# Performance work log

Hardware: AMD Instinct MI355X
Metric: run time of the kernel (lower is better)

## Reference

```python
import jax, jax.numpy as jnp
import numpy as np


def setup_inputs() -> dict:
    key = jax.random.key(0)
    k1, k2 = jax.random.split(key)
    B, M, N = 4, 8192, 8192
    pc_src = jax.random.normal(k1, (B, 3, M), dtype=jnp.float32)
    pc_dst = jax.random.normal(k2, (B, 3, N), dtype=jnp.float32)
    return {"pc_src": pc_src, "pc_dst": pc_dst}


def reference(pc_src, pc_dst):
    # pc_src: [B, 3, M], pc_dst: [B, 3, N]
    # Pairwise squared L2 via ||a||^2 + ||b||^2 - 2 a.b (avoids [B,3,M,N] diff tensor)
    src_sq = jnp.sum(pc_src * pc_src, axis=1)          # [B, M]
    dst_sq = jnp.sum(pc_dst * pc_dst, axis=1)          # [B, N]
    cross = jnp.einsum('bdm,bdn->bmn', pc_src, pc_dst)  # [B, M, N]
    d2 = src_sq[:, :, None] + dst_sq[:, None, :] - 2.0 * cross
    dist = jnp.sqrt(jnp.maximum(d2, 0.0))               # [B, M, N]
    min_dist = jnp.min(dist, axis=2)                     # [B, M]
    return jnp.mean(min_dist)
```

## Files before the change

kernel.cpp:

```cpp
#include <hip/hip_runtime.h>
#include <math.h>


#define TPB 256

constexpr int NB = 4;
constexpr int NM = 8192;
constexpr int NN = 8192;
constexpr int NPTS = NB * NM;
constexpr int NSEG = 16;
constexpr int DSEG = NN / NSEG;
constexpr int TILES = DSEG / 32;
constexpr int NSRCG = NM / 512;
constexpr int FIN_TPB = 128;
constexpr int NBLK_F = NPTS / FIN_TPB;

typedef _Float16 half8 __attribute__((ext_vector_type(8)));
typedef float f32x16 __attribute__((ext_vector_type(16)));

__device__ __forceinline__ float min3(float a, float b, float c) {
    return fminf(fminf(a, b), c);
}
__device__ __forceinline__ float tile_min(const f32x16& c, float acc) {
    float v0 = min3(c[0],  c[1],  c[2]);
    float v1 = min3(c[3],  c[4],  c[5]);
    float v2 = min3(c[6],  c[7],  c[8]);
    float v3 = min3(c[9],  c[10], c[11]);
    float v4 = min3(c[12], c[13], c[14]);
    float w0 = min3(v0, v1, c[15]);
    float w1 = min3(v2, v3, v4);
    return min3(acc, w0, w1);
}
__device__ __forceinline__ int aidx(int r, int h) {
    return ((r << 1) | h) ^ ((r >> 2) & 7);
}

__global__ __launch_bounds__(TPB) void minseg_kernel(const float* __restrict__ src,
                                                     const float* __restrict__ dst,
                                                     float* __restrict__ part,
                                                     unsigned long long* __restrict__ sumfix,
                                                     unsigned* __restrict__ ticket) {
    __shared__ uint4 alds[DSEG * 2];

    int l  = threadIdx.x & 63;
    int wv = threadIdx.x >> 6;
    int sg = blockIdx.x & (NSEG - 1);
    int b  = (blockIdx.x >> 4) & 3;
    int srcgrp = blockIdx.x >> 6;

    if (blockIdx.x == 0 && threadIdx.x == 0) { *sumfix = 0ULL; *ticket = 0u; }

    const float* pd = dst + (size_t)b * 3 * NN;
#pragma unroll
    for (int rr = 0; rr < 2; ++rr) {
        int r = threadIdx.x + rr * TPB;
        int n = sg * DSEG + r;
        float x = pd[n], y = pd[NN + n], z = pd[2 * NN + n];
        float ux = -2.0f * x, uy = -2.0f * y, uz = -2.0f * z;
        float w = fmaf(x, x, fmaf(y, y, z * z));
        _Float16 uhx = (_Float16)ux; _Float16 ulx = (_Float16)(ux - (float)uhx);
        _Float16 uhy = (_Float16)uy; _Float16 uly = (_Float16)(uy - (float)uhy);
        _Float16 uhz = (_Float16)uz; _Float16 ulz = (_Float16)(uz - (float)uhz);
        _Float16 wh  = (_Float16)w;  _Float16 wl  = (_Float16)(w - (float)wh);
        half8 a0 = {uhx, uhx, ulx, uhy, uhy, uly, uhz, uhz};
        half8 a1 = {ulz, wh, wl, (_Float16)0.f, (_Float16)0.f,
                    (_Float16)0.f, (_Float16)0.f, (_Float16)0.f};
        alds[aidx(r, 0)] = *(uint4*)&a0;
        alds[aidx(r, 1)] = *(uint4*)&a1;
    }

    int mbase = (srcgrp * 4 + wv) * 128;
    int lg = l & 31;
    int hi = l >> 5;
    const float* ps = src + (size_t)b * 3 * NM;
    half8 bf[4];
#pragma unroll
    for (int k = 0; k < 4; ++k) {
        int c = mbase + k * 32 + lg;
        float x = ps[c], y = ps[NM + c], z = ps[2 * NM + c];
        _Float16 shx = (_Float16)x; _Float16 slx = (_Float16)(x - (float)shx);
        _Float16 shy = (_Float16)y; _Float16 sly = (_Float16)(y - (float)shy);
        _Float16 shz = (_Float16)z; _Float16 slz = (_Float16)(z - (float)shz);
        half8 b0 = {shx, slx, shx, shy, sly, shy, shz, slz};
        half8 b1 = {shz, (_Float16)1.f, (_Float16)1.f, (_Float16)0.f,
                    (_Float16)0.f, (_Float16)0.f, (_Float16)0.f, (_Float16)0.f};
        bf[k] = hi ? b1 : b0;
    }
    __syncthreads();

    const f32x16 zc = {0.f,0.f,0.f,0.f,0.f,0.f,0.f,0.f,
                       0.f,0.f,0.f,0.f,0.f,0.f,0.f,0.f};
    float acc0 = 3.4e38f, acc1 = 3.4e38f, acc2 = 3.4e38f, acc3 = 3.4e38f;
#pragma unroll 2
    for (int j = 0; j < TILES; ++j) {
        uint4 av = alds[aidx(j * 32 + lg, hi)];
        half8 af = *(half8*)&av;
        f32x16 c0 = __builtin_amdgcn_mfma_f32_32x32x16_f16(af, bf[0], zc, 0, 0, 0);
        acc0 = tile_min(c0, acc0);
        f32x16 c1 = __builtin_amdgcn_mfma_f32_32x32x16_f16(af, bf[1], zc, 0, 0, 0);
        acc1 = tile_min(c1, acc1);
        f32x16 c2 = __builtin_amdgcn_mfma_f32_32x32x16_f16(af, bf[2], zc, 0, 0, 0);
        acc2 = tile_min(c2, acc2);
        f32x16 c3 = __builtin_amdgcn_mfma_f32_32x32x16_f16(af, bf[3], zc, 0, 0, 0);
        acc3 = tile_min(c3, acc3);
    }

    acc0 = fminf(acc0, __shfl_xor(acc0, 32));
    acc1 = fminf(acc1, __shfl_xor(acc1, 32));
    acc2 = fminf(acc2, __shfl_xor(acc2, 32));
    acc3 = fminf(acc3, __shfl_xor(acc3, 32));

    float* pp = part + (size_t)sg * NPTS + b * NM + mbase;
    int lo = (l < 32);
    pp[lo ? lg      : 32 + lg] = lo ? acc0 : acc1;
    pp[lo ? 64 + lg : 96 + lg] = lo ? acc2 : acc3;
}

__global__ __launch_bounds__(FIN_TPB) void finish_kernel(const float* __restrict__ src,
                                                         const float* __restrict__ part,
                                                         unsigned long long* __restrict__ sumfix,
                                                         unsigned* __restrict__ ticket,
                                                         float* __restrict__ out) {
    int gm = blockIdx.x * FIN_TPB + threadIdx.x;
    int b = gm / NM, m = gm % NM;

    float v = fminf(part[gm], part[NPTS + gm]);
#pragma unroll
    for (int s = 2; s < NSEG; s += 2)
        v = min3(v, part[(size_t)s * NPTS + gm], part[(size_t)(s + 1) * NPTS + gm]);

    const float* sp = src + (size_t)b * 3 * NM;
    float x = sp[m], y = sp[NM + m], z = sp[2 * NM + m];
    float a2 = fmaf(x, x, fmaf(y, y, z * z));
    float d = sqrtf(fmaxf(a2 + v, 0.0f));

    for (int off = 32; off > 0; off >>= 1) d += __shfl_down(d, off);
    __shared__ float wsum[2];
    int lane = threadIdx.x & 63, w = threadIdx.x >> 6;
    if (lane == 0) wsum[w] = d;
    __syncthreads();

    if (threadIdx.x == 0) {
        float bs = wsum[0] + wsum[1];
        unsigned long long inc = (unsigned long long)((double)bs * 4294967296.0);
        atomicAdd(sumfix, inc);
        __threadfence();
        unsigned tk = atomicAdd(ticket, 1u);
        if (tk == NBLK_F - 1) {
            unsigned long long tot = atomicAdd(sumfix, 0ULL);
            out[0] = (float)((double)tot * (1.0 / 4294967296.0) * (1.0 / NPTS));
        }
    }
}

extern "C" void kernel_launch(void* const* d_in, const int* in_sizes, int n_in,
                              void* d_out, int out_size, void* d_ws, size_t ws_size,
                              hipStream_t stream) {
    const float* src = (const float*)d_in[0];
    const float* dst = (const float*)d_in[1];
    float* out = (float*)d_out;

    char* ws = (char*)d_ws;
    float* part = (float*)ws;
    unsigned long long* sumfix =
        (unsigned long long*)(ws + (size_t)NSEG * NPTS * 4);
    unsigned* ticket = (unsigned*)(ws + (size_t)NSEG * NPTS * 4 + 8);

    minseg_kernel<<<NSEG * NB * NSRCG, TPB, 0, stream>>>(src, dst, part,
                                                         sumfix, ticket);
    finish_kernel<<<NBLK_F, FIN_TPB, 0, stream>>>(src, part, sumfix, ticket, out);
}
```

Baseline: 27.62 us.

## Fuse finish reduction into min kernel via per-group last-block tickets

Result: slower. 94.72 us (+243.0%).

```diff
diff --git a/kernel.cpp b/kernel.cpp
--- a/kernel.cpp
+++ b/kernel.cpp
@@ -12,8 +12,7 @@
 constexpr int DSEG = NN / NSEG;
 constexpr int TILES = DSEG / 32;
 constexpr int NSRCG = NM / 512;
-constexpr int FIN_TPB = 128;
-constexpr int NBLK_F = NPTS / FIN_TPB;
+constexpr int NGRP = NB * NSRCG;
 
 typedef _Float16 half8 __attribute__((ext_vector_type(8)));
 typedef float f32x16 __attribute__((ext_vector_type(16)));
@@ -35,20 +34,22 @@
     return ((r << 1) | h) ^ ((r >> 2) & 7);
 }
 
-__global__ __launch_bounds__(TPB) void minseg_kernel(const float* __restrict__ src,
-                                                     const float* __restrict__ dst,
-                                                     float* __restrict__ part,
-                                                     unsigned long long* __restrict__ sumfix,
-                                                     unsigned* __restrict__ ticket) {
+__global__ __launch_bounds__(TPB) void fused_kernel(const float* __restrict__ src,
+                                                    const float* __restrict__ dst,
+                                                    float* __restrict__ part,
+                                                    unsigned* __restrict__ tg,
+                                                    unsigned long long* __restrict__ sumfix,
+                                                    unsigned* __restrict__ ticket,
+                                                    float* __restrict__ out) {
     __shared__ uint4 alds[DSEG * 2];
+    __shared__ int sfold;
+    __shared__ float wsum[4];
 
     int l  = threadIdx.x & 63;
     int wv = threadIdx.x >> 6;
     int sg = blockIdx.x & (NSEG - 1);
     int b  = (blockIdx.x >> 4) & 3;
     int srcgrp = blockIdx.x >> 6;
-
-    if (blockIdx.x == 0 && threadIdx.x == 0) { *sumfix = 0ULL; *ticket = 0u; }
 
     const float* pd = dst + (size_t)b * 3 * NN;
 #pragma unroll
@@ -112,41 +113,57 @@
 
     float* pp = part + (size_t)sg * NPTS + b * NM + mbase;
     int lo = (l < 32);
-    pp[lo ? lg      : 32 + lg] = lo ? acc0 : acc1;
-    pp[lo ? 64 + lg : 96 + lg] = lo ? acc2 : acc3;
-}
-
-__global__ __launch_bounds__(FIN_TPB) void finish_kernel(const float* __restrict__ src,
-                                                         const float* __restrict__ part,
-                                                         unsigned long long* __restrict__ sumfix,
-                                                         unsigned* __restrict__ ticket,
-                                                         float* __restrict__ out) {
-    int gm = blockIdx.x * FIN_TPB + threadIdx.x;
-    int b = gm / NM, m = gm % NM;
-
-    float v = fminf(part[gm], part[NPTS + gm]);
-#pragma unroll
-    for (int s = 2; s < NSEG; s += 2)
-        v = min3(v, part[(size_t)s * NPTS + gm], part[(size_t)(s + 1) * NPTS + gm]);
-
-    const float* sp = src + (size_t)b * 3 * NM;
-    float x = sp[m], y = sp[NM + m], z = sp[2 * NM + m];
-    float a2 = fmaf(x, x, fmaf(y, y, z * z));
-    float d = sqrtf(fmaxf(a2 + v, 0.0f));
-
-    for (int off = 32; off > 0; off >>= 1) d += __shfl_down(d, off);
-    __shared__ float wsum[2];
-    int lane = threadIdx.x & 63, w = threadIdx.x >> 6;
-    if (lane == 0) wsum[w] = d;
+    __hip_atomic_store(&pp[lo ? lg : 32 + lg], lo ? acc0 : acc1,
+                       __ATOMIC_RELAXED, __HIP_MEMORY_SCOPE_AGENT);
+    __hip_atomic_store(&pp[lo ? 64 + lg : 96 + lg], lo ? acc2 : acc3,
+                       __ATOMIC_RELAXED, __HIP_MEMORY_SCOPE_AGENT);
+    __threadfence();
     __syncthreads();
 
     if (threadIdx.x == 0) {
-        float bs = wsum[0] + wsum[1];
+        unsigned old = __hip_atomic_fetch_add(&tg[b * NSRCG + srcgrp], 1u,
+                                              __ATOMIC_ACQ_REL,
+                                              __HIP_MEMORY_SCOPE_AGENT);
+        sfold = (old == NSEG - 1);
+    }
+    __syncthreads();
+    if (!sfold) return;
+
+    int gbase = b * NM + srcgrp * 512;
+    const float* sp = src + (size_t)b * 3 * NM;
+    float dsum = 0.0f;
+#pragma unroll
+    for (int cc = 0; cc < 2; ++cc) {
+        int c = threadIdx.x + cc * TPB;
+        int gm = gbase + c;
+        float v = fminf(
+            __hip_atomic_load(&part[gm], __ATOMIC_RELAXED, __HIP_MEMORY_SCOPE_AGENT),
+            __hip_atomic_load(&part[NPTS + gm], __ATOMIC_RELAXED, __HIP_MEMORY_SCOPE_AGENT));
+#pragma unroll
+        for (int s = 2; s < NSEG; s += 2) {
+            float va = __hip_atomic_load(&part[(size_t)s * NPTS + gm],
+                                         __ATOMIC_RELAXED, __HIP_MEMORY_SCOPE_AGENT);
+            float vb = __hip_atomic_load(&part[(size_t)(s + 1) * NPTS + gm],
+                                         __ATOMIC_RELAXED, __HIP_MEMORY_SCOPE_AGENT);
+            v = min3(v, va, vb);
+        }
+        int m = srcgrp * 512 + c;
+        float x = sp[m], y = sp[NM + m], z = sp[2 * NM + m];
+        float a2 = fmaf(x, x, fmaf(y, y, z * z));
+        dsum += sqrtf(fmaxf(a2 + v, 0.0f));
+    }
+
+    for (int off = 32; off > 0; off >>= 1) dsum += __shfl_down(dsum, off);
+    if (l == 0) wsum[wv] = dsum;
+    __syncthreads();
+
+    if (threadIdx.x == 0) {
+        float bs = (wsum[0] + wsum[1]) + (wsum[2] + wsum[3]);
         unsigned long long inc = (unsigned long long)((double)bs * 4294967296.0);
         atomicAdd(sumfix, inc);
         __threadfence();
         unsigned tk = atomicAdd(ticket, 1u);
-        if (tk == NBLK_F - 1) {
+        if (tk == NGRP - 1) {
             unsigned long long tot = atomicAdd(sumfix, 0ULL);
             out[0] = (float)((double)tot * (1.0 / 4294967296.0) * (1.0 / NPTS));
         }
@@ -162,11 +179,12 @@
 
     char* ws = (char*)d_ws;
     float* part = (float*)ws;
-    unsigned long long* sumfix =
-        (unsigned long long*)(ws + (size_t)NSEG * NPTS * 4);
-    unsigned* ticket = (unsigned*)(ws + (size_t)NSEG * NPTS * 4 + 8);
+    char* ctrl = ws + (size_t)NSEG * NPTS * 4;
+    unsigned* tg = (unsigned*)ctrl;
+    unsigned long long* sumfix = (unsigned long long*)(ctrl + 256);
+    unsigned* ticket = (unsigned*)(ctrl + 264);
 
-    minseg_kernel<<<NSEG * NB * NSRCG, TPB, 0, stream>>>(src, dst, part,
-                                                         sumfix, ticket);
-    finish_kernel<<<NBLK_F, FIN_TPB, 0, stream>>>(src, part, sumfix, ticket, out);
+    hipMemsetAsync(ctrl, 0, 272, stream);
+    fused_kernel<<<NSEG * NB * NSRCG, TPB, 0, stream>>>(src, dst, part, tg,
+                                                        sumfix, ticket, out);
 }
```

## Replace atomic ticket reduction with per-block sums and a final reduce kernel

Applied to the files above, without the earlier changes.

After: 23.40 us, median of 2. 15.3% less time.

```diff
diff --git a/kernel.cpp b/kernel.cpp
--- a/kernel.cpp
+++ b/kernel.cpp
@@ -12,7 +12,7 @@
 constexpr int DSEG = NN / NSEG;
 constexpr int TILES = DSEG / 32;
 constexpr int NSRCG = NM / 512;
-constexpr int FIN_TPB = 128;
+constexpr int FIN_TPB = 256;
 constexpr int NBLK_F = NPTS / FIN_TPB;
 
 typedef _Float16 half8 __attribute__((ext_vector_type(8)));
@@ -37,9 +37,7 @@
 
 __global__ __launch_bounds__(TPB) void minseg_kernel(const float* __restrict__ src,
                                                      const float* __restrict__ dst,
-                                                     float* __restrict__ part,
-                                                     unsigned long long* __restrict__ sumfix,
-                                                     unsigned* __restrict__ ticket) {
+                                                     float* __restrict__ part) {
     __shared__ uint4 alds[DSEG * 2];
 
     int l  = threadIdx.x & 63;
@@ -47,8 +45,6 @@
     int sg = blockIdx.x & (NSEG - 1);
     int b  = (blockIdx.x >> 4) & 3;
     int srcgrp = blockIdx.x >> 6;
-
-    if (blockIdx.x == 0 && threadIdx.x == 0) { *sumfix = 0ULL; *ticket = 0u; }
 
     const float* pd = dst + (size_t)b * 3 * NN;
 #pragma unroll
@@ -96,12 +92,12 @@
         uint4 av = alds[aidx(j * 32 + lg, hi)];
         half8 af = *(half8*)&av;
         f32x16 c0 = __builtin_amdgcn_mfma_f32_32x32x16_f16(af, bf[0], zc, 0, 0, 0);
+        f32x16 c1 = __builtin_amdgcn_mfma_f32_32x32x16_f16(af, bf[1], zc, 0, 0, 0);
+        f32x16 c2 = __builtin_amdgcn_mfma_f32_32x32x16_f16(af, bf[2], zc, 0, 0, 0);
+        f32x16 c3 = __builtin_amdgcn_mfma_f32_32x32x16_f16(af, bf[3], zc, 0, 0, 0);
         acc0 = tile_min(c0, acc0);
-        f32x16 c1 = __builtin_amdgcn_mfma_f32_32x32x16_f16(af, bf[1], zc, 0, 0, 0);
         acc1 = tile_min(c1, acc1);
-        f32x16 c2 = __builtin_amdgcn_mfma_f32_32x32x16_f16(af, bf[2], zc, 0, 0, 0);
         acc2 = tile_min(c2, acc2);
-        f32x16 c3 = __builtin_amdgcn_mfma_f32_32x32x16_f16(af, bf[3], zc, 0, 0, 0);
         acc3 = tile_min(c3, acc3);
     }
 
@@ -118,9 +114,7 @@
 
 __global__ __launch_bounds__(FIN_TPB) void finish_kernel(const float* __restrict__ src,
                                                          const float* __restrict__ part,
-                                                         unsigned long long* __restrict__ sumfix,
-                                                         unsigned* __restrict__ ticket,
-                                                         float* __restrict__ out) {
+                                                         float* __restrict__ bsums) {
     int gm = blockIdx.x * FIN_TPB + threadIdx.x;
     int b = gm / NM, m = gm % NM;
 
@@ -135,22 +129,24 @@
     float d = sqrtf(fmaxf(a2 + v, 0.0f));
 
     for (int off = 32; off > 0; off >>= 1) d += __shfl_down(d, off);
-    __shared__ float wsum[2];
+    __shared__ float wsum[4];
     int lane = threadIdx.x & 63, w = threadIdx.x >> 6;
     if (lane == 0) wsum[w] = d;
     __syncthreads();
+    if (threadIdx.x == 0)
+        bsums[blockIdx.x] = (wsum[0] + wsum[1]) + (wsum[2] + wsum[3]);
+}
 
-    if (threadIdx.x == 0) {
-        float bs = wsum[0] + wsum[1];
-        unsigned long long inc = (unsigned long long)((double)bs * 4294967296.0);
-        atomicAdd(sumfix, inc);
-        __threadfence();
-        unsigned tk = atomicAdd(ticket, 1u);
-        if (tk == NBLK_F - 1) {
-            unsigned long long tot = atomicAdd(sumfix, 0ULL);
-            out[0] = (float)((double)tot * (1.0 / 4294967296.0) * (1.0 / NPTS));
-        }
-    }
+__global__ __launch_bounds__(TPB) void final_kernel(const float* __restrict__ bsums,
+                                                    float* __restrict__ out) {
+    float v = (threadIdx.x < NBLK_F) ? bsums[threadIdx.x] : 0.0f;
+    for (int off = 32; off > 0; off >>= 1) v += __shfl_down(v, off);
+    __shared__ float wsum[4];
+    int lane = threadIdx.x & 63, w = threadIdx.x >> 6;
+    if (lane == 0) wsum[w] = v;
+    __syncthreads();
+    if (threadIdx.x == 0)
+        out[0] = ((wsum[0] + wsum[1]) + (wsum[2] + wsum[3])) * (1.0f / NPTS);
 }
 
 extern "C" void kernel_launch(void* const* d_in, const int* in_sizes, int n_in,
@@ -161,12 +157,10 @@
     float* out = (float*)d_out;
 
     char* ws = (char*)d_ws;
-    float* part = (float*)ws;
-    unsigned long long* sumfix =
-        (unsigned long long*)(ws + (size_t)NSEG * NPTS * 4);
-    unsigned* ticket = (unsigned*)(ws + (size_t)NSEG * NPTS * 4 + 8);
+    float* part  = (float*)ws;
+    float* bsums = (float*)(ws + (size_t)NSEG * NPTS * 4);
 
-    minseg_kernel<<<NSEG * NB * NSRCG, TPB, 0, stream>>>(src, dst, part,
-                                                         sumfix, ticket);
-    finish_kernel<<<NBLK_F, FIN_TPB, 0, stream>>>(src, part, sumfix, ticket, out);
+    minseg_kernel<<<NSEG * NB * NSRCG, TPB, 0, stream>>>(src, dst, part);
+    finish_kernel<<<NBLK_F, FIN_TPB, 0, stream>>>(src, part, bsums);
+    final_kernel<<<1, TPB, 0, stream>>>(bsums, out);
 }
```
